# Kernel tuning notes

Hardware: AMD Instinct MI355X
Metric: run time of the kernel (lower is better)

The kernel has to match this reference:

```python
import jax, jax.numpy as jnp
import numpy as np

EPS = 1e-5

def adain_norm(x):
    # per-(batch,channel) instance normalization over spatial dims (AdaIN projection)
    mean = jnp.mean(x, axis=(2, 3), keepdims=True)
    var = jnp.var(x, axis=(2, 3), keepdims=True)
    return (x - mean) / jnp.sqrt(var + EPS)

def conv1x1(x, w, b):
    # x: [B,C,H,W], w: [O,C], b: [O]
    return jnp.einsum('bchw,oc->bohw', x, w) + b[None, :, None, None]

def setup_inputs() -> dict:
    key = jax.random.key(0)
    ks = jax.random.split(key, 10)
    B, C, H, W = 4, 512, 64, 64
    s = 1.0 / np.sqrt(C)
    return {
        'x': jax.random.normal(ks[0], (B, C, H, W), jnp.float32),
        'y': jax.random.normal(ks[1], (B, C, H, W), jnp.float32),
        'f_w': jax.random.normal(ks[2], (C, C), jnp.float32) * s,
        'f_b': jnp.zeros((C,), jnp.float32),
        'g_w': jax.random.normal(ks[3], (C, C), jnp.float32) * s,
        'g_b': jnp.zeros((C,), jnp.float32),
        'h_w': jax.random.normal(ks[4], (C, C), jnp.float32) * s,
        'h_b': jnp.zeros((C,), jnp.float32),
        'out_w': jax.random.normal(ks[5], (C, C), jnp.float32) * s,
        'out_b': jnp.zeros((C,), jnp.float32),
    }

def reference(x, y, f_w, f_b, g_w, g_b, h_w, h_b, out_w, out_b):
    B, C, H, W = x.shape
    HW = H * W
    xn = adain_norm(x)
    yn = adain_norm(y)
    # 1x1 conv projections, flattened over spatial dims
    f = conv1x1(xn, f_w, f_b).reshape(B, C, HW)   # [B,C,HWx]
    g = conv1x1(yn, g_w, g_b).reshape(B, C, HW)   # [B,C,HWy]
    energy = jnp.einsum('bci,bcj->bij', f, g)     # [B,HWx,HWy]
    correlation = jax.nn.softmax(energy, axis=-1)
    h = conv1x1(y, h_w, h_b).reshape(B, C, HW)    # [B,C,HWy]
    # residual = h @ correlation^T -> [B,C,HWx]
    residual = jnp.einsum('bcj,bij->bci', h, correlation).reshape(B, C, H, W)
    residual = conv1x1(residual, out_w, out_b)
    return x + residual
```

## Files before the change

### kernel.cpp

```cpp
#include <hip/hip_runtime.h>
#include <stdint.h>

#define HW 4096
#define NC 512
#define NB 4

typedef __attribute__((ext_vector_type(8))) _Float16 f16x8;
typedef __attribute__((ext_vector_type(4))) float f32x4;
typedef __attribute__((ext_vector_type(4))) unsigned short ush4;
typedef __attribute__((ext_vector_type(8))) unsigned short ush8;

typedef __attribute__((address_space(1))) const void* as1_cvp;
typedef __attribute__((address_space(3))) void* as3_vp;

__device__ __forceinline__ unsigned short f2h(float f) {
  union { _Float16 h; unsigned short u; } c;
  c.h = (_Float16)f;
  return c.u;
}

__global__ __launch_bounds__(256) void moments_k(const float* __restrict__ x,
                                                 const float* __restrict__ y,
                                                 float* __restrict__ stats) {
  int bid = blockIdx.x;
  int tens = bid >> 11;
  int row = bid & 2047;
  const float* src = (tens ? y : x) + (size_t)row * HW;
  float s = 0.f, s2 = 0.f;
  for (int j = threadIdx.x; j < HW / 4; j += 256) {
    float4 v = ((const float4*)src)[j];
    s += (v.x + v.y) + (v.z + v.w);
    s2 += (v.x * v.x + v.y * v.y) + (v.z * v.z + v.w * v.w);
  }
  #pragma unroll
  for (int o = 32; o; o >>= 1) { s += __shfl_down(s, o); s2 += __shfl_down(s2, o); }
  __shared__ float rs[8];
  int w = threadIdx.x >> 6;
  if ((threadIdx.x & 63) == 0) { rs[w] = s; rs[4 + w] = s2; }
  __syncthreads();
  if (threadIdx.x == 0) {
    float S = (rs[0] + rs[1]) + (rs[2] + rs[3]);
    float S2 = (rs[4] + rs[5]) + (rs[6] + rs[7]);
    float mean = S * (1.f / HW);
    float var = S2 * (1.f / HW) - mean * mean;
    stats[tens * 4096 + row] = mean;
    stats[tens * 4096 + 2048 + row] = rsqrtf(var + 1e-5f);
  }
}

__global__ __launch_bounds__(256) void transnorm_k(const float* __restrict__ x,
                                                   const float* __restrict__ y,
                                                   const float* __restrict__ stats,
                                                   unsigned short* __restrict__ xnT,
                                                   unsigned short* __restrict__ ynT,
                                                   unsigned short* __restrict__ yT) {
  __shared__ float tile[64][65];
  int zi = blockIdx.z;
  int b = zi / 3, mode = zi - b * 3;
  int i0 = blockIdx.x * 64, c0 = blockIdx.y * 64;
  const float* src = (mode == 0 ? x : y);
  unsigned short* dst = (mode == 0 ? xnT : (mode == 1 ? ynT : yT));
  int t = threadIdx.x;
  int c = t >> 2;
  int isub = (t & 3) << 4;
  float mean = 0.f, rstd = 1.f;
  if (mode < 2) {
    int srow = (mode ? 4096 : 0) + b * NC + c0 + c;
    mean = stats[srow];
    rstd = stats[srow + 2048];
  }
  const float4* sp = (const float4*)(src + ((size_t)(b * NC + c0 + c)) * HW + i0 + isub);
  #pragma unroll
  for (int k = 0; k < 4; ++k) {
    float4 v = sp[k];
    int ib = isub + k * 4;
    tile[ib + 0][c] = (v.x - mean) * rstd;
    tile[ib + 1][c] = (v.y - mean) * rstd;
    tile[ib + 2][c] = (v.z - mean) * rstd;
    tile[ib + 3][c] = (v.w - mean) * rstd;
  }
  __syncthreads();
  int i = t >> 2;
  int cc = (t & 3) << 4;
  unsigned short* op = dst + ((size_t)b * HW + i0 + i) * NC + c0 + cc;
  #pragma unroll
  for (int h = 0; h < 2; ++h) {
    ush8 o;
    #pragma unroll
    for (int e = 0; e < 8; ++e) o[e] = f2h(tile[i][cc + h * 8 + e]);
    *(ush8*)(op + h * 8) = o;
  }
}

__global__ __launch_bounds__(256) void castw_k(const float* __restrict__ fw,
                                               const float* __restrict__ gw,
                                               const float* __restrict__ hw_,
                                               const float* __restrict__ ow,
                                               unsigned short* __restrict__ dst) {
  int idx = blockIdx.x * 256 + threadIdx.x;
  int which = idx >> 16;
  int sub = idx & 65535;
  const float* s = which == 0 ? fw : which == 1 ? gw : which == 2 ? hw_ : ow;
  float4 v = ((const float4*)s)[sub];
  ush4 o;
  o[0] = f2h(v.x); o[1] = f2h(v.y); o[2] = f2h(v.z); o[3] = f2h(v.w);
  *(ush4*)(dst + (size_t)idx * 4) = o;
}

__global__ __launch_bounds__(256) void softmax_k(float* __restrict__ S) {
  float* row = S + (size_t)blockIdx.x * HW;
  int t = threadIdx.x;
  float4 v[4];
  float mx = -3.0e38f;
  #pragma unroll
  for (int r = 0; r < 4; ++r) {
    v[r] = ((const float4*)row)[r * 256 + t];
    mx = fmaxf(mx, fmaxf(fmaxf(v[r].x, v[r].y), fmaxf(v[r].z, v[r].w)));
  }
  #pragma unroll
  for (int o = 32; o; o >>= 1) mx = fmaxf(mx, __shfl_down(mx, o));
  __shared__ float red[8];
  int w = t >> 6;
  if ((t & 63) == 0) red[w] = mx;
  __syncthreads();
  mx = fmaxf(fmaxf(red[0], red[1]), fmaxf(red[2], red[3]));
  float sum = 0.f;
  #pragma unroll
  for (int r = 0; r < 4; ++r) {
    v[r].x = __expf(v[r].x - mx);
    v[r].y = __expf(v[r].y - mx);
    v[r].z = __expf(v[r].z - mx);
    v[r].w = __expf(v[r].w - mx);
    sum += (v[r].x + v[r].y) + (v[r].z + v[r].w);
  }
  #pragma unroll
  for (int o = 32; o; o >>= 1) sum += __shfl_down(sum, o);
  if ((t & 63) == 0) red[4 + w] = sum;
  __syncthreads();
  float inv = 1.f / ((red[4] + red[5]) + (red[6] + red[7]));
  unsigned short* orow = (unsigned short*)row;
  #pragma unroll
  for (int r = 0; r < 4; ++r) {
    ush4 o;
    o[0] = f2h(v[r].x * inv);
    o[1] = f2h(v[r].y * inv);
    o[2] = f2h(v[r].z * inv);
    o[3] = f2h(v[r].w * inv);
    *(ush4*)(orow + ((size_t)(r * 256 + t)) * 4) = o;
  }
}

__global__ __launch_bounds__(256) void reduce_k(const float* __restrict__ S,
                                                unsigned short* __restrict__ op,
                                                long long PSo, int nsplit, int R, int pzs) {
  int e = blockIdx.x * 256 + threadIdx.x;
  int bg = e >> pzs;
  int rem = e - (bg << pzs);
  int m = rem >> 7;
  int c4 = rem & 127;
  const float* rowp = S + (size_t)bg * R * HW + (size_t)m * HW + 2048 + c4 * 4;
  float4 s = {0.f, 0.f, 0.f, 0.f};
  for (int sp = 0; sp < nsplit; ++sp) {
    float4 v = *(const float4*)(rowp + sp * 512);
    s.x += v.x; s.y += v.y; s.z += v.z; s.w += v.w;
  }
  ush4 o;
  o[0] = f2h(s.x); o[1] = f2h(s.y); o[2] = f2h(s.z); o[3] = f2h(s.w);
  *(ush4*)(op + (size_t)bg * PSo + (size_t)m * NC + c4 * 4) = o;
}

__global__ __launch_bounds__(256) void gemm_nt(
    const unsigned short* __restrict__ A, long long sA, int lda,
    const unsigned short* __restrict__ Bm, long long sB, int ldb,
    void* __restrict__ Cp, long long sC, long long sCs, int ldc,
    int K, int out_f32, int ls,
    const float* __restrict__ bias_m, const float* __restrict__ bias_n,
    const float* __restrict__ add_src, long long sAdd) {
  __shared__ short lsA[128 * 64];
  __shared__ short lsB[128 * 64];
  const int t = threadIdx.x;
  const int lane = t & 63;
  const int w = t >> 6;
  const int wm = w >> 1, wn = w & 1;
  const long long bz = blockIdx.z;
  const long long bg = bz >> ls;
  const int sp = (int)(bz - (bg << ls));
  const long long koff = (long long)sp * K;
  const unsigned short* Ab = A + bg * sA + koff + (size_t)blockIdx.x * 128 * lda;
  const unsigned short* Bb = Bm + bg * sB + koff + (size_t)blockIdx.y * 128 * ldb;

  f32x4 zero = {0.f, 0.f, 0.f, 0.f};
  f32x4 acc[4][4];
  #pragma unroll
  for (int i = 0; i < 4; ++i)
    #pragma unroll
    for (int j = 0; j < 4; ++j) acc[i][j] = zero;

  const int nkt = K >> 6;
  for (int kt = 0; kt < nkt; ++kt) {
    const int kbase = kt << 6;
    #pragma unroll
    for (int i = 0; i < 4; ++i) {
      int q = t + i * 256;
      int r = q >> 3, xx = q & 7;
      int gk = kbase + ((xx ^ (r & 7)) << 3);
      __builtin_amdgcn_global_load_lds((as1_cvp)(const void*)(Ab + (size_t)r * lda + gk),
                                       (as3_vp)(void*)(&lsA[q << 3]), 16, 0, 0);
      __builtin_amdgcn_global_load_lds((as1_cvp)(const void*)(Bb + (size_t)r * ldb + gk),
                                       (as3_vp)(void*)(&lsB[q << 3]), 16, 0, 0);
    }
    __syncthreads();
    #pragma unroll
    for (int ks = 0; ks < 2; ++ks) {
      f16x8 av[4], bv[4];
      const int xl = ks * 4 + (lane >> 4);
      const int rr = lane & 15;
      #pragma unroll
      for (int mb = 0; mb < 4; ++mb) {
        int row = wm * 64 + mb * 16 + rr;
        av[mb] = *(const f16x8*)&lsA[(row << 6) + ((xl ^ (row & 7)) << 3)];
      }
      #pragma unroll
      for (int nb = 0; nb < 4; ++nb) {
        int row = wn * 64 + nb * 16 + rr;
        bv[nb] = *(const f16x8*)&lsB[(row << 6) + ((xl ^ (row & 7)) << 3)];
      }
      #pragma unroll
      for (int mb = 0; mb < 4; ++mb)
        #pragma unroll
        for (int nb = 0; nb < 4; ++nb)
          acc[mb][nb] = __builtin_amdgcn_mfma_f32_16x16x32_f16(av[mb], bv[nb], acc[mb][nb], 0, 0, 0);
    }
    __syncthreads();
  }

  const int mb0 = blockIdx.x * 128 + wm * 64;
  const int nb0 = blockIdx.y * 128 + wn * 64;
  const int cn = lane & 15;
  const int rq = (lane >> 4) << 2;
  float* cf = (float*)Cp;
  unsigned short* ch = (unsigned short*)Cp;
  #pragma unroll
  for (int mb = 0; mb < 4; ++mb) {
    #pragma unroll
    for (int nb = 0; nb < 4; ++nb) {
      int n = nb0 + nb * 16 + cn;
      float bn = bias_n ? bias_n[n] : 0.f;
      #pragma unroll
      for (int r = 0; r < 4; ++r) {
        int m = mb0 + mb * 16 + rq + r;
        float vv = acc[mb][nb][r] + bn;
        if (bias_m) vv += bias_m[m];
        if (add_src) vv += add_src[bg * sAdd + (size_t)m * ldc + n];
        size_t off = (size_t)(bg * sC) + (size_t)sp * sCs + (size_t)m * ldc + n;
        if (out_f32) cf[off] = vv;
        else ch[off] = f2h(vv);
      }
    }
  }
}

__global__ __launch_bounds__(512, 2) void gemm_nt2(
    const unsigned short* __restrict__ A, long long sA, int lda,
    const unsigned short* __restrict__ Bm, long long sB, int ldb,
    void* __restrict__ Cp, long long sC, long long sCs, int ldc,
    int K, int out_f32, int ls,
    const float* __restrict__ bias_n) {
  __shared__ short lsA[2][256 * 64];
  __shared__ short lsB[2][256 * 64];
  const int t = threadIdx.x;
  const int lane = t & 63;
  const int w = t >> 6;
  const int wm = w >> 2, wn = w & 3;
  const long long bz = blockIdx.z;
  const long long bg = bz >> ls;
  const int sp = (int)(bz - (bg << ls));
  const long long koff = (long long)sp * K;
  const unsigned short* Ab = A + bg * sA + koff + (size_t)blockIdx.x * 256 * lda;
  const unsigned short* Bb = Bm + bg * sB + koff + (size_t)blockIdx.y * 256 * ldb;

  f32x4 zero = {0.f, 0.f, 0.f, 0.f};
  f32x4 acc[8][4];
  #pragma unroll
  for (int i = 0; i < 8; ++i)
    #pragma unroll
    for (int j = 0; j < 4; ++j) acc[i][j] = zero;

  const int rr = lane & 15;
  const int xl = lane >> 4;
  const int nkt = K >> 6;

  auto STAGE = [&](int buf, int kt) {
    const int kbase = kt << 6;
    #pragma unroll
    for (int i = 0; i < 4; ++i) {
      int q = t + i * 512;
      int r = q >> 3, xx = q & 7;
      int gk = kbase + ((xx ^ (r & 7)) << 3);
      __builtin_amdgcn_global_load_lds((as1_cvp)(const void*)(Ab + (size_t)r * lda + gk),
                                       (as3_vp)(void*)(&lsA[buf][q << 3]), 16, 0, 0);
      __builtin_amdgcn_global_load_lds((as1_cvp)(const void*)(Bb + (size_t)r * ldb + gk),
                                       (as3_vp)(void*)(&lsB[buf][q << 3]), 16, 0, 0);
    }
  };

  STAGE(0, 0);
  __syncthreads();
  int cur = 0;
  for (int kt = 0; kt < nkt; ++kt) {
    if (kt + 1 < nkt) STAGE(cur ^ 1, kt + 1);
    #pragma unroll
    for (int ks = 0; ks < 2; ++ks) {
      f16x8 av[8], bv[4];
      const int cb = ks * 4 + xl;
      #pragma unroll
      for (int mb = 0; mb < 8; ++mb) {
        int row = wm * 128 + mb * 16 + rr;
        av[mb] = *(const f16x8*)&lsA[cur][(row << 6) + ((cb ^ (row & 7)) << 3)];
      }
      #pragma unroll
      for (int nb = 0; nb < 4; ++nb) {
        int row = wn * 64 + nb * 16 + rr;
        bv[nb] = *(const f16x8*)&lsB[cur][(row << 6) + ((cb ^ (row & 7)) << 3)];
      }
      __builtin_amdgcn_s_setprio(1);
      #pragma unroll
      for (int mb = 0; mb < 8; ++mb)
        #pragma unroll
        for (int nb = 0; nb < 4; ++nb)
          acc[mb][nb] = __builtin_amdgcn_mfma_f32_16x16x32_f16(av[mb], bv[nb], acc[mb][nb], 0, 0, 0);
      __builtin_amdgcn_s_setprio(0);
    }
    __syncthreads();
    cur ^= 1;
  }

  const int mb0 = blockIdx.x * 256 + wm * 128;
  const int nb0 = blockIdx.y * 256 + wn * 64;
  const int cn = lane & 15;
  const int rq = (lane >> 4) << 2;
  float* cf = (float*)Cp;
  unsigned short* ch = (unsigned short*)Cp;
  #pragma unroll
  for (int mb = 0; mb < 8; ++mb) {
    #pragma unroll
    for (int nb = 0; nb < 4; ++nb) {
      int n = nb0 + nb * 16 + cn;
      float bn = bias_n ? bias_n[n] : 0.f;
      #pragma unroll
      for (int r = 0; r < 4; ++r) {
        int m = mb0 + mb * 16 + rq + r;
        float vv = acc[mb][nb][r] + bn;
        size_t off = (size_t)(bg * sC) + (size_t)sp * sCs + (size_t)m * ldc + n;
        if (out_f32) cf[off] = vv;
        else ch[off] = f2h(vv);
      }
    }
  }
}

extern "C" void kernel_launch(void* const* d_in, const int* in_sizes, int n_in,
                              void* d_out, int out_size, void* d_ws, size_t ws_size,
                              hipStream_t stream) {
  const float* x = (const float*)d_in[0];
  const float* y = (const float*)d_in[1];
  const float* f_w = (const float*)d_in[2];
  const float* f_b = (const float*)d_in[3];
  const float* g_w = (const float*)d_in[4];
  const float* g_b = (const float*)d_in[5];
  const float* h_w = (const float*)d_in[6];
  const float* h_b = (const float*)d_in[7];
  const float* out_w = (const float*)d_in[8];
  const float* out_b = (const float*)d_in[9];
  float* out = (float*)d_out;

  char* ws = (char*)d_ws;
  size_t off = 0;
  auto alloc = [&](size_t bytes) -> char* {
    char* p = ws + off;
    off += (bytes + 255) & ~(size_t)255;
    return p;
  };
  const size_t TN = (size_t)NB * HW * NC;
  float* stats = (float*)alloc(8192 * sizeof(float));
  unsigned short* wB = (unsigned short*)alloc((size_t)4 * 512 * 512 * 2);
  unsigned short* xnT = (unsigned short*)alloc(TN * 2);
  unsigned short* ynT = (unsigned short*)alloc(TN * 2);
  unsigned short* yT = (unsigned short*)alloc(TN * 2);
  unsigned short* fB = (unsigned short*)alloc(TN * 2);
  unsigned short* gB = (unsigned short*)alloc(TN * 2);
  unsigned short* hB = (unsigned short*)alloc(TN * 2);
  unsigned short* oB = xnT;
  size_t remain = ws_size > off ? ws_size - off : 0;
  const size_t SB = (size_t)HW * HW * 4;
  int G, R = HW;
  if (remain >= 4 * SB)      { G = 4; }
  else if (remain >= 2 * SB) { G = 2; }
  else if (remain >= SB)     { G = 1; }
  else {
    G = 1;
    while (R > 128 && (size_t)R * HW * 4 > remain) R >>= 1;
  }
  float* S = (float*)alloc((size_t)G * R * HW * 4);
  if (off > ws_size) return;

  castw_k<<<dim3(1024), dim3(256), 0, stream>>>(f_w, g_w, h_w, out_w, wB);
  moments_k<<<dim3(4096), dim3(256), 0, stream>>>(x, y, stats);
  transnorm_k<<<dim3(64, 8, 12), dim3(256), 0, stream>>>(x, y, stats, xnT, ynT, yT);

  const long long PS = (long long)HW * NC;
  gemm_nt<<<dim3(32, 4, NB), dim3(256), 0, stream>>>(xnT, PS, NC, wB, 0, NC,
                                                     fB, PS, 0, NC, NC, 0, 0,
                                                     nullptr, f_b, nullptr, 0);
  gemm_nt<<<dim3(32, 4, NB), dim3(256), 0, stream>>>(ynT, PS, NC, wB + 262144, 0, NC,
                                                     gB, PS, 0, NC, NC, 0, 0,
                                                     nullptr, g_b, nullptr, 0);
  gemm_nt<<<dim3(4, 32, NB), dim3(256), 0, stream>>>(wB + 524288, 0, NC, yT, PS, NC,
                                                     hB, PS, 0, HW, NC, 0, 0,
                                                     h_b, nullptr, nullptr, 0);

  const int pzs = 31 - __builtin_clz((unsigned)(R * (NC / 4)));
  for (int b0 = 0; b0 < NB; b0 += G) {
    for (int r0 = 0; r0 < HW; r0 += R) {
      if (R >= 256) {
        gemm_nt2<<<dim3(R / 256, HW / 256, G), dim3(512), 0, stream>>>(
            fB + ((size_t)b0 * HW + r0) * NC, PS, NC,
            gB + (size_t)b0 * PS, PS, NC,
            S, (long long)R * HW, 0, HW, NC, 1, 0, nullptr);
        softmax_k<<<dim3(G * R), dim3(256), 0, stream>>>(S);
        gemm_nt2<<<dim3(R / 256, NC / 256, G * 4), dim3(512), 0, stream>>>(
            (const unsigned short*)S, (long long)R * 2 * HW, 2 * HW,
            hB + (size_t)b0 * NC * HW, (long long)NC * HW, HW,
            S + 2048, (long long)R * HW, 512, HW, HW / 4, 1, 2, nullptr);
        reduce_k<<<dim3(G * R / 2), dim3(256), 0, stream>>>(
            S, oB + ((size_t)b0 * HW + r0) * NC, PS, 4, R, pzs);
      } else {
        gemm_nt<<<dim3(R / 128, 32, G), dim3(256), 0, stream>>>(
            fB + ((size_t)b0 * HW + r0) * NC, PS, NC,
            gB + (size_t)b0 * PS, PS, NC,
            S, (long long)R * HW, 0, HW, NC, 1, 0, nullptr, nullptr, nullptr, 0);
        softmax_k<<<dim3(G * R), dim3(256), 0, stream>>>(S);
        gemm_nt<<<dim3(R / 128, 4, G * 4), dim3(256), 0, stream>>>(
            (const unsigned short*)S, (long long)R * 2 * HW, 2 * HW,
            hB + (size_t)b0 * NC * HW, (long long)NC * HW, HW,
            S + 2048, (long long)R * HW, 512, HW, HW / 4, 1, 2,
            nullptr, nullptr, nullptr, 0);
        reduce_k<<<dim3(G * R / 2), dim3(256), 0, stream>>>(
            S, oB + ((size_t)b0 * HW + r0) * NC, PS, 4, R, pzs);
      }
    }
  }
  gemm_nt<<<dim3(4, 32, NB), dim3(256), 0, stream>>>(wB + 786432, 0, NC, oB, PS, NC,
                                                     out, (long long)NC * HW, 0, HW, NC, 1, 0,
                                                     out_b, nullptr, x, (long long)NC * HW);
}
```

Before: 446.5 us.

## Fuse y normalize/cast in transpose and move projections to 256-tile GEMM

The transpose kernel now reads y once and writes both the normalized and raw fp16 transposes, so y is no longer loaded twice. Per-channel mean and rstd go into shared memory. The f and g projections are merged into one gemm_nt2 launch, which switches the B operand and bias by blockIdx.z. The h and output projections also move to the larger 256x256 gemm_nt2 kernel, which gains bias_m and residual-add epilogue support. The aim is fewer launches, less redundant global traffic and better MFMA tile efficiency, at the cost of fewer blocks for these mid-sized GEMMs.

```diff
diff --git a/kernel.cpp b/kernel.cpp
--- a/kernel.cpp
+++ b/kernel.cpp
@@ -55,40 +55,58 @@
                                                    unsigned short* __restrict__ ynT,
                                                    unsigned short* __restrict__ yT) {
   __shared__ float tile[64][65];
+  __shared__ float ms[64], rsd[64];
   int zi = blockIdx.z;
-  int b = zi / 3, mode = zi - b * 3;
+  int b = zi >> 1, mode = zi & 1;
   int i0 = blockIdx.x * 64, c0 = blockIdx.y * 64;
-  const float* src = (mode == 0 ? x : y);
-  unsigned short* dst = (mode == 0 ? xnT : (mode == 1 ? ynT : yT));
+  const float* src = mode ? y : x;
   int t = threadIdx.x;
   int c = t >> 2;
   int isub = (t & 3) << 4;
-  float mean = 0.f, rstd = 1.f;
-  if (mode < 2) {
-    int srow = (mode ? 4096 : 0) + b * NC + c0 + c;
-    mean = stats[srow];
-    rstd = stats[srow + 2048];
+  if (t < 64) {
+    int srow = (mode ? 4096 : 0) + b * NC + c0 + t;
+    ms[t] = stats[srow];
+    rsd[t] = stats[srow + 2048];
   }
   const float4* sp = (const float4*)(src + ((size_t)(b * NC + c0 + c)) * HW + i0 + isub);
   #pragma unroll
   for (int k = 0; k < 4; ++k) {
     float4 v = sp[k];
     int ib = isub + k * 4;
-    tile[ib + 0][c] = (v.x - mean) * rstd;
-    tile[ib + 1][c] = (v.y - mean) * rstd;
-    tile[ib + 2][c] = (v.z - mean) * rstd;
-    tile[ib + 3][c] = (v.w - mean) * rstd;
+    tile[ib + 0][c] = v.x;
+    tile[ib + 1][c] = v.y;
+    tile[ib + 2][c] = v.z;
+    tile[ib + 3][c] = v.w;
   }
   __syncthreads();
   int i = t >> 2;
   int cc = (t & 3) << 4;
-  unsigned short* op = dst + ((size_t)b * HW + i0 + i) * NC + c0 + cc;
-  #pragma unroll
-  for (int h = 0; h < 2; ++h) {
-    ush8 o;
-    #pragma unroll
-    for (int e = 0; e < 8; ++e) o[e] = f2h(tile[i][cc + h * 8 + e]);
-    *(ush8*)(op + h * 8) = o;
+  size_t obase = ((size_t)b * HW + i0 + i) * NC + c0 + cc;
+  if (mode == 0) {
+    #pragma unroll
+    for (int h = 0; h < 2; ++h) {
+      ush8 o;
+      #pragma unroll
+      for (int e = 0; e < 8; ++e) {
+        int ce = cc + h * 8 + e;
+        o[e] = f2h((tile[i][ce] - ms[ce]) * rsd[ce]);
+      }
+      *(ush8*)(xnT + obase + h * 8) = o;
+    }
+  } else {
+    #pragma unroll
+    for (int h = 0; h < 2; ++h) {
+      ush8 on,or_;
+      #pragma unroll
+      for (int e = 0; e < 8; ++e) {
+        int ce = cc + h * 8 + e;
+        float raw = tile[i][ce];
+        on[e] = f2h((raw - ms[ce]) * rsd[ce]);
+        or_[e] = f2h(raw);
+      }
+      *(ush8*)(ynT + obase + h * 8) = on;
+      *(ush8*)(yT + obase + h * 8) = or_;
+    }
   }
 }
 
@@ -265,7 +283,10 @@
     const unsigned short* __restrict__ Bm, long long sB, int ldb,
     void* __restrict__ Cp, long long sC, long long sCs, int ldc,
     int K, int out_f32, int ls,
-    const float* __restrict__ bias_n) {
+    const float* __restrict__ bias_m, const float* __restrict__ bias_n,
+    const float* __restrict__ add_src, long long sAdd,
+    const unsigned short* __restrict__ B2, const float* __restrict__ bias_n2,
+    int zsw) {
   __shared__ short lsA[2][256 * 64];
   __shared__ short lsB[2][256 * 64];
   const int t = threadIdx.x;
@@ -273,10 +294,12 @@
   const int w = t >> 6;
   const int wm = w >> 2, wn = w & 3;
   const long long bz = blockIdx.z;
+  if ((int)bz >= zsw) { Bm = B2; bias_n = bias_n2; }
   const long long bg = bz >> ls;
   const int sp = (int)(bz - (bg << ls));
   const long long koff = (long long)sp * K;
-  const unsigned short* Ab = A + bg * sA + koff + (size_t)blockIdx.x * 256 * lda;
+  const unsigned short* Ab = A + bz * (ls ? 0 : sA) + (ls ? bg * sA : 0) + koff
+                           + (size_t)blockIdx.x * 256 * lda;
   const unsigned short* Bb = Bm + bg * sB + koff + (size_t)blockIdx.y * 256 * ldb;
 
   f32x4 zero = {0.f, 0.f, 0.f, 0.f};
@@ -351,6 +374,8 @@
       for (int r = 0; r < 4; ++r) {
         int m = mb0 + mb * 16 + rq + r;
         float vv = acc[mb][nb][r] + bn;
+        if (bias_m) vv += bias_m[m];
+        if (add_src) vv += add_src[bg * sAdd + (size_t)m * ldc + n];
         size_t off = (size_t)(bg * sC) + (size_t)sp * sCs + (size_t)m * ldc + n;
         if (out_f32) cf[off] = vv;
         else ch[off] = f2h(vv);
@@ -406,18 +431,16 @@
 
   castw_k<<<dim3(1024), dim3(256), 0, stream>>>(f_w, g_w, h_w, out_w, wB);
   moments_k<<<dim3(4096), dim3(256), 0, stream>>>(x, y, stats);
-  transnorm_k<<<dim3(64, 8, 12), dim3(256), 0, stream>>>(x, y, stats, xnT, ynT, yT);
+  transnorm_k<<<dim3(64, 8, 8), dim3(256), 0, stream>>>(x, y, stats, xnT, ynT, yT);
 
   const long long PS = (long long)HW * NC;
-  gemm_nt<<<dim3(32, 4, NB), dim3(256), 0, stream>>>(xnT, PS, NC, wB, 0, NC,
-                                                     fB, PS, 0, NC, NC, 0, 0,
-                                                     nullptr, f_b, nullptr, 0);
-  gemm_nt<<<dim3(32, 4, NB), dim3(256), 0, stream>>>(ynT, PS, NC, wB + 262144, 0, NC,
-                                                     gB, PS, 0, NC, NC, 0, 0,
-                                                     nullptr, g_b, nullptr, 0);
-  gemm_nt<<<dim3(4, 32, NB), dim3(256), 0, stream>>>(wB + 524288, 0, NC, yT, PS, NC,
-                                                     hB, PS, 0, HW, NC, 0, 0,
-                                                     h_b, nullptr, nullptr, 0);
+  const int BIG = 1 << 30;
+  gemm_nt2<<<dim3(16, 2, 8), dim3(512), 0, stream>>>(
+      xnT, PS, NC, wB, 0, NC, fB, PS, 0, NC, NC, 0, 0,
+      nullptr, f_b, nullptr, 0, wB + 262144, g_b, 4);
+  gemm_nt2<<<dim3(2, 16, NB), dim3(512), 0, stream>>>(
+      wB + 524288, 0, NC, yT, PS, NC, hB, PS, 0, HW, NC, 0, 0,
+      h_b, nullptr, nullptr, 0, wB, nullptr, BIG);
 
   const int pzs = 31 - __builtin_clz((unsigned)(R * (NC / 4)));
   for (int b0 = 0; b0 < NB; b0 += G) {
@@ -426,12 +449,14 @@
         gemm_nt2<<<dim3(R / 256, HW / 256, G), dim3(512), 0, stream>>>(
             fB + ((size_t)b0 * HW + r0) * NC, PS, NC,
             gB + (size_t)b0 * PS, PS, NC,
-            S, (long long)R * HW, 0, HW, NC, 1, 0, nullptr);
+            S, (long long)R * HW, 0, HW, NC, 1, 0,
+            nullptr, nullptr, nullptr, 0, wB, nullptr, BIG);
         softmax_k<<<dim3(G * R), dim3(256), 0, stream>>>(S);
         gemm_nt2<<<dim3(R / 256, NC / 256, G * 4), dim3(512), 0, stream>>>(
             (const unsigned short*)S, (long long)R * 2 * HW, 2 * HW,
             hB + (size_t)b0 * NC * HW, (long long)NC * HW, HW,
-            S + 2048, (long long)R * HW, 512, HW, HW / 4, 1, 2, nullptr);
+            S + 2048, (long long)R * HW, 512, HW, HW / 4, 1, 2,
+            nullptr, nullptr, nullptr, 0, wB, nullptr, BIG);
         reduce_k<<<dim3(G * R / 2), dim3(256), 0, stream>>>(
             S, oB + ((size_t)b0 * HW + r0) * NC, PS, 4, R, pzs);
       } else {
@@ -450,7 +475,8 @@
       }
     }
   }
-  gemm_nt<<<dim3(4, 32, NB), dim3(256), 0, stream>>>(wB + 786432, 0, NC, oB, PS, NC,
-                                                     out, (long long)NC * HW, 0, HW, NC, 1, 0,
-                                                     out_b, nullptr, x, (long long)NC * HW);
-}
+  gemm_nt2<<<dim3(2, 16, NB), dim3(512), 0, stream>>>(
+      wB + 786432, 0, NC, oB, PS, NC,
+      out, (long long)NC * HW, 0, HW, NC, 1, 0,
+      out_b, nullptr, x, (long long)NC * HW, wB, nullptr, BIG);
+}
```

After: 504.9 us. 13.1% more time.
